# Optimization experiments

Hardware: AMD Instinct MI355X
Metric: run time of the kernel (lower is better)

The kernel has to match this reference:

```python
import jax, jax.numpy as jnp
import numpy as np

DIM = 1024
NUM_HEADS = 32
HEAD_DIM = 32
T = 2048
SCALE = 0.12
ROT_BASE = HEAD_DIM * 4  # Rotary(head_dim, max_seq_len, head_dim*4)
RMS_EPS = 1.1920929e-07  # torch float32 finfo eps (F.rms_norm default)


def _rms_norm(x):
    ms = jnp.mean(jnp.square(x), axis=-1, keepdims=True)
    return x * jax.lax.rsqrt(ms + RMS_EPS)


def _rotary_tables(seq_len):
    # modded-nanogpt half-truncated rotary: frequencies on first quarter, zeros on second
    quarter = HEAD_DIM // 4
    af = (1.0 / ROT_BASE) ** jnp.linspace(0.0, 1.0, quarter, dtype=jnp.float32)
    af = jnp.concatenate([af, jnp.zeros(quarter, dtype=jnp.float32)])  # [hd/2]
    theta = jnp.arange(seq_len, dtype=jnp.float32)[:, None] * af[None, :]  # [T, hd/2]
    return jnp.cos(theta), jnp.sin(theta)


def _apply_rotary(x, cos, sin):
    # x: [B, T, H, hd]; cos/sin: [T, hd/2]
    x1, x2 = jnp.split(x, 2, axis=-1)
    c = cos[None, :, None, :]
    s = sin[None, :, None, :]
    y1 = x1 * c + x2 * s
    y2 = -x1 * s + x2 * c
    return jnp.concatenate([y1, y2], axis=-1)


def setup_inputs() -> dict:
    key = jax.random.key(0)
    k1, k2, k3, k4 = jax.random.split(key, 4)
    std = 0.5 * DIM ** (-0.5)
    bound = (3.0 ** 0.5) * std
    x = jax.random.normal(k1, (1, T, DIM), dtype=jnp.float32)
    ve = jax.random.normal(k2, (1, T, NUM_HEADS * HEAD_DIM), dtype=jnp.float32)
    qkv_w = jax.random.uniform(k3, (3, NUM_HEADS * HEAD_DIM, DIM), dtype=jnp.float32,
                               minval=-bound, maxval=bound)
    lambdas = jnp.array([0.5, 0.5], dtype=jnp.float32)
    # original zero-inits c_proj; use small random so output/grads are nontrivial
    c_proj_w = jax.random.normal(k4, (DIM, NUM_HEADS * HEAD_DIM), dtype=jnp.float32) * 0.02
    return {"x": x, "ve": ve, "qkv_w": qkv_w, "lambdas": lambdas, "c_proj_w": c_proj_w}


def reference(x, ve, qkv_w, lambdas, c_proj_w):
    B, T_, D = x.shape
    H, hd = NUM_HEADS, HEAD_DIM
    # fused QKV projection: F.linear(x, qkv_w.flatten(end_dim=1))
    w = qkv_w.reshape(3 * H * hd, D)
    qkv = jnp.einsum('btd,ed->bte', x, w).reshape(B, T_, 3 * H, hd)
    q, k, v = jnp.split(qkv, 3, axis=2)  # each [B, T, H, hd]
    q = _rms_norm(q)
    k = _rms_norm(k)
    cos, sin = _rotary_tables(T_)
    q = _apply_rotary(q, cos, sin)
    k = _apply_rotary(k, cos, sin)
    v = lambdas[0] * v + lambdas[1] * ve.reshape(B, T_, H, hd)
    # causal attention with fixed scale 0.12
    scores = jnp.einsum('bqhd,bkhd->bhqk', q, k) * SCALE
    causal = jnp.tril(jnp.ones((T_, T_), dtype=bool))
    scores = jnp.where(causal[None, None, :, :], scores, -jnp.inf)
    attn = jax.nn.softmax(scores, axis=-1)
    y = jnp.einsum('bhqk,bkhd->bqhd', attn, v).reshape(B, T_, H * hd)
    return jnp.einsum('bte,de->btd', y, c_proj_w)
```

## Files before the change

kernel.cpp:

```cpp
#include <hip/hip_runtime.h>
#include <hip/hip_bf16.h>

#define NHEADS 32
#define HD_ 32
#define TSEQ 2048
#define SCALE_ 0.12f
#define LOG2E_ 1.44269504088896f
#define RMS_EPS_ 1.1920929e-07f

typedef unsigned short ushort_t;
typedef __bf16 bf16_t;
typedef __attribute__((ext_vector_type(8))) bf16_t bf16x8;
typedef __attribute__((ext_vector_type(4))) float f32x4;
typedef __attribute__((ext_vector_type(8))) unsigned short u16x8;

__device__ __forceinline__ ushort_t f2bfn(float f){
    __hip_bfloat16 b = __float2bfloat16(f);
    return *reinterpret_cast<ushort_t*>(&b);
}
__device__ __forceinline__ float bf2f(ushort_t s){
    union { unsigned u; float f; } v; v.u = ((unsigned)s) << 16;
    return v.f;
}
__device__ __forceinline__ float fexp2(float x){
#if __has_builtin(__builtin_amdgcn_exp2f)
    return __builtin_amdgcn_exp2f(x);
#else
    return exp2f(x);
#endif
}
__device__ __forceinline__ void gld16(const void* g, void* l){
    __builtin_amdgcn_global_load_lds(
        (const __attribute__((address_space(1))) unsigned int*)g,
        (__attribute__((address_space(3))) unsigned int*)l,
        16, 0, 0);
}

__global__ __launch_bounds__(256) void k_convert(const float* __restrict__ src,
                                                 ushort_t* __restrict__ dst, int n4){
    int i = blockIdx.x * blockDim.x + threadIdx.x;
    int stride = gridDim.x * blockDim.x;
    for (; i < n4; i += stride){
        float4 v = ((const float4*)src)[i];
        ushort4 o;
        o.x = f2bfn(v.x); o.y = f2bfn(v.y); o.z = f2bfn(v.z); o.w = f2bfn(v.w);
        ((ushort4*)dst)[i] = o;
    }
}

__global__ __launch_bounds__(256) void k_tables(float* __restrict__ cost, float* __restrict__ sint){
    int gid = blockIdx.x * 256 + threadIdx.x;
    if (gid >= TSEQ * 16) return;
    int t = gid >> 4, i = gid & 15;
    float c = 1.0f, s = 0.0f;
    if (i < 8){
        float af = powf(1.0f / 128.0f, (float)i * (1.0f / 7.0f));
        float th = (float)t * af;
        sincosf(th, &s, &c);
    }
    cost[gid] = c;
    sint[gid] = s;
}

template<int BM, int BN, bool OUT_BF16>
__global__ __launch_bounds__(256) void k_gemm64(const ushort_t* __restrict__ A,
                                                const ushort_t* __restrict__ B,
                                                void* __restrict__ C,
                                                int M, int N, int K)
{
    constexpr int MI = BM / 32, NI = BN / 32;
    __shared__ __align__(16) ushort_t As[BM * 64];
    __shared__ __align__(16) ushort_t Bs[BN * 64];
    const int tid = threadIdx.x;
    const int lane = tid & 63;
    const int w = tid >> 6;
    const int wr = w >> 1, wc = w & 1;
    const int l15 = lane & 15, hi = lane >> 4;
    const int m0 = blockIdx.y * BM, n0 = blockIdx.x * BN;
    const int srow = lane >> 3, scol = (lane & 7) * 8;

    f32x4 acc[MI][NI] = {};

    for (int k0 = 0; k0 < K; k0 += 64){
        __syncthreads();
        #pragma unroll
        for (int i = 0; i < BM / 32; ++i){
            int c = w * (BM / 32) + i;
            gld16(&A[(size_t)(m0 + c * 8 + srow) * K + k0 + scol], &As[c * 512]);
        }
        #pragma unroll
        for (int i = 0; i < BN / 32; ++i){
            int c = w * (BN / 32) + i;
            gld16(&B[(size_t)(n0 + c * 8 + srow) * K + k0 + scol], &Bs[c * 512]);
        }
        __syncthreads();
        bf16x8 af[MI][2], bfr[NI][2];
        #pragma unroll
        for (int mi = 0; mi < MI; ++mi)
            #pragma unroll
            for (int sub = 0; sub < 2; ++sub)
                af[mi][sub] = *(const bf16x8*)&As[(wr * (BM/2) + mi * 16 + l15) * 64 + sub * 32 + hi * 8];
        #pragma unroll
        for (int ni = 0; ni < NI; ++ni)
            #pragma unroll
            for (int sub = 0; sub < 2; ++sub)
                bfr[ni][sub] = *(const bf16x8*)&Bs[(wc * (BN/2) + ni * 16 + l15) * 64 + sub * 32 + hi * 8];
        #pragma unroll
        for (int sub = 0; sub < 2; ++sub)
            #pragma unroll
            for (int mi = 0; mi < MI; ++mi)
                #pragma unroll
                for (int ni = 0; ni < NI; ++ni)
                    acc[mi][ni] = __builtin_amdgcn_mfma_f32_16x16x32_bf16(af[mi][sub], bfr[ni][sub], acc[mi][ni], 0, 0, 0);
    }

    #pragma unroll
    for (int mi = 0; mi < MI; ++mi)
        #pragma unroll
        for (int ni = 0; ni < NI; ++ni)
            #pragma unroll
            for (int r = 0; r < 4; ++r){
                int row = m0 + wr * (BM/2) + mi * 16 + hi * 4 + r;
                int col = n0 + wc * (BN/2) + ni * 16 + l15;
                float v = acc[mi][ni][r];
                if (OUT_BF16) ((ushort_t*)C)[(size_t)row * N + col] = f2bfn(v);
                else          ((float*)C)[(size_t)row * N + col] = v;
            }
}

__global__ __launch_bounds__(256) void k_fuse(const ushort_t* __restrict__ qkvb,
                                              const float* __restrict__ ve,
                                              const float* __restrict__ lam,
                                              const float* __restrict__ cost,
                                              const float* __restrict__ sint,
                                              ushort_t* __restrict__ qb,
                                              ushort_t* __restrict__ kb,
                                              ushort_t* __restrict__ vtb)
{
    const int h  = blockIdx.y;
    const int t0 = blockIdx.x * 64;
    const int tid = threadIdx.x;
    const int tl = tid >> 2;
    const int dg = tid & 3;
    const int t  = t0 + tl;

    __shared__ __align__(16) float vtile[32 * 65];

    float cs[8], sn[8];
    #pragma unroll
    for (int j = 0; j < 8; ++j){
        int ci = (dg * 8 + j) & 15;
        cs[j] = cost[t * 16 + ci];
        sn[j] = sint[t * 16 + ci];
    }
    const float sgn = (dg < 2) ? 1.0f : -1.0f;

    #pragma unroll
    for (int which = 0; which < 2; ++which){
        u16x8 raw = *(const u16x8*)&qkvb[(size_t)t * 3072 + which * 1024 + h * 32 + dg * 8];
        float v[8];
        float ss = 0.0f;
        #pragma unroll
        for (int j = 0; j < 8; ++j){ v[j] = bf2f(raw[j]); ss += v[j] * v[j]; }
        ss += __shfl_xor(ss, 1);
        ss += __shfl_xor(ss, 2);
        const float inv = rsqrtf(ss * (1.0f / 32.0f) + RMS_EPS_);
        const float scl = (which == 0) ? SCALE_ * LOG2E_ : 1.0f;
        u16x8 o;
        #pragma unroll
        for (int j = 0; j < 8; ++j){
            float nv = v[j] * inv;
            float p  = __shfl_xor(nv, 2);
            o[j] = f2bfn((nv * cs[j] + sgn * p * sn[j]) * scl);
        }
        ushort_t* dst = (which == 0) ? qb : kb;
        *(u16x8*)&dst[((size_t)h * TSEQ + t) * 32 + dg * 8] = o;
    }

    const float l0 = lam[0], l1 = lam[1];
    {
        u16x8 raw = *(const u16x8*)&qkvb[(size_t)t * 3072 + 2048 + h * 32 + dg * 8];
        const float4* vep = (const float4*)&ve[(size_t)t * 1024 + h * 32 + dg * 8];
        float4 a = vep[0], b = vep[1];
        float vef[8] = {a.x, a.y, a.z, a.w, b.x, b.y, b.z, b.w};
        #pragma unroll
        for (int j = 0; j < 8; ++j)
            vtile[(dg * 8 + j) * 65 + tl] = l0 * bf2f(raw[j]) + l1 * vef[j];
    }
    __syncthreads();
    {
        const int d = tid >> 3, jj = tid & 7;
        u16x8 o;
        #pragma unroll
        for (int e = 0; e < 8; ++e)
            o[e] = f2bfn(vtile[d * 65 + jj * 8 + e]);
        *(u16x8*)&vtb[((size_t)h * HD_ + d) * TSEQ + t0 + jj * 8] = o;
    }
}

struct ChainState { f32x4 a0, a1; float m, lp; };

template<bool MASK>
__device__ __forceinline__ void attn_tile(const ushort_t* __restrict__ kb_h,
                                          const ushort_t* __restrict__ vt_h,
                                          ushort_t* pb, const bf16x8& qf,
                                          int kb0, int qglob, int l15, int hi,
                                          ChainState& st)
{
    bf16x8 vv0[2], vv1[2];
    #pragma unroll
    for (int kk = 0; kk < 2; ++kk){
        vv0[kk] = *(const bf16x8*)&vt_h[(size_t)l15 * TSEQ + kb0 + kk * 32 + hi * 8];
        vv1[kk] = *(const bf16x8*)&vt_h[(size_t)(16 + l15) * TSEQ + kb0 + kk * 32 + hi * 8];
    }
    f32x4 s[4];
    #pragma unroll
    for (int ni = 0; ni < 4; ++ni){
        bf16x8 kf = *(const bf16x8*)&kb_h[(size_t)(kb0 + ni * 16 + l15) * 32 + hi * 8];
        f32x4 z = {0.f, 0.f, 0.f, 0.f};
        s[ni] = __builtin_amdgcn_mfma_f32_16x16x32_bf16(kf, qf, z, 0, 0, 0);
    }
    if (MASK){
        #pragma unroll
        for (int ni = 0; ni < 4; ++ni)
            #pragma unroll
            for (int r = 0; r < 4; ++r)
                if (kb0 + ni * 16 + hi * 4 + r > qglob) s[ni][r] = -1e30f;
    }
    float mt = -1e30f;
    #pragma unroll
    for (int ni = 0; ni < 4; ++ni)
        #pragma unroll
        for (int r = 0; r < 4; ++r)
            mt = fmaxf(mt, s[ni][r]);
    mt = fmaxf(mt, __shfl_xor(mt, 16));
    mt = fmaxf(mt, __shfl_xor(mt, 32));
    float mn = fmaxf(st.m, mt);
    float sc = fexp2(st.m - mn);
    st.m = mn;
    float ps = 0.f;
    #pragma unroll
    for (int ni = 0; ni < 4; ++ni)
        #pragma unroll
        for (int r = 0; r < 4; ++r){
            float p = fexp2(s[ni][r] - mn);
            s[ni][r] = p;
            ps += p;
        }
    st.lp = st.lp * sc + ps;
    #pragma unroll
    for (int r = 0; r < 4; ++r){ st.a0[r] *= sc; st.a1[r] *= sc; }
    #pragma unroll
    for (int ni = 0; ni < 4; ++ni){
        ushort4 pk;
        pk.x = f2bfn(s[ni][0]); pk.y = f2bfn(s[ni][1]);
        pk.z = f2bfn(s[ni][2]); pk.w = f2bfn(s[ni][3]);
        *(ushort4*)&pb[l15 * 72 + ni * 16 + hi * 4] = pk;
    }
    #pragma unroll
    for (int kk = 0; kk < 2; ++kk){
        bf16x8 pf = *(const bf16x8*)&pb[l15 * 72 + kk * 32 + hi * 8];
        st.a0 = __builtin_amdgcn_mfma_f32_16x16x32_bf16(vv0[kk], pf, st.a0, 0, 0, 0);
        st.a1 = __builtin_amdgcn_mfma_f32_16x16x32_bf16(vv1[kk], pf, st.a1, 0, 0, 0);
    }
}

__device__ __forceinline__ void run_range(const ushort_t* kb_h, const ushort_t* vt_h,
                                          ushort_t* pb, const bf16x8& qf, int qglob,
                                          int lo, int hi_t, int nT, int l15, int hi,
                                          ChainState& st)
{
    int stop = (hi_t < nT) ? hi_t : (nT - 1);
    for (int kt = lo; kt < stop; ++kt)
        attn_tile<false>(kb_h, vt_h, pb, qf, kt * 64, qglob, l15, hi, st);
    if (hi_t == nT && lo < nT)
        attn_tile<true>(kb_h, vt_h, pb, qf, (nT - 1) * 64, qglob, l15, hi, st);
}

__device__ __forceinline__ void merge_state(ChainState& s, const float* mb){
    float m2 = mb[0];
    float mn = fmaxf(s.m, m2);
    float f1 = fexp2(s.m - mn), f2 = fexp2(m2 - mn);
    s.lp = s.lp * f1 + mb[1] * f2;
    #pragma unroll
    for (int r = 0; r < 4; ++r){
        s.a0[r] = s.a0[r] * f1 + mb[2 + r] * f2;
        s.a1[r] = s.a1[r] * f1 + mb[6 + r] * f2;
    }
    s.m = mn;
}

__global__ __launch_bounds__(512, 4) void k_attn(const ushort_t* __restrict__ qb,
                                                 const ushort_t* __restrict__ kb,
                                                 const ushort_t* __restrict__ vtb,
                                                 ushort_t* __restrict__ yb)
{
    const int h  = blockIdx.y;
    const int b  = blockIdx.x;
    const int tid = threadIdx.x;
    const int w = tid >> 6, lane = tid & 63;
    const int ws = w & 3, half2 = w >> 2;
    const int l15 = lane & 15, hi = lane >> 4;

    __shared__ __align__(16) ushort_t Pall[8][16 * 72];
    __shared__ float mbuf[4][64][20];
    ushort_t* pb = &Pall[w][0];

    const ushort_t* kb_h = kb + (size_t)h * TSEQ * HD_;
    const ushort_t* vt_h = vtb + (size_t)h * HD_ * TSEQ;
    const ushort_t* qb_h = qb + (size_t)h * TSEQ * HD_;

    const int qtA = b, qtB = 31 - b;
    const int nA = qtA + 1, nB = qtB + 1;
    const int hA = (nA + 1) >> 1, hB = nB >> 1;

    const int qwA = qtA * 64 + ws * 16;
    const int qwB = qtB * 64 + ws * 16;
    const bf16x8 qfA = *(const bf16x8*)&qb_h[(size_t)(qwA + l15) * 32 + hi * 8];
    const bf16x8 qfB = *(const bf16x8*)&qb_h[(size_t)(qwB + l15) * 32 + hi * 8];

    ChainState stA, stB;
    stA.a0 = {0.f,0.f,0.f,0.f}; stA.a1 = {0.f,0.f,0.f,0.f}; stA.m = -1e30f; stA.lp = 0.f;
    stB = stA;

    if (half2 == 0){
        run_range(kb_h, vt_h, pb, qfA, qwA + l15, 0, hA, nA, l15, hi, stA);
        run_range(kb_h, vt_h, pb, qfB, qwB + l15, 0, hB, nB, l15, hi, stB);
    } else {
        run_range(kb_h, vt_h, pb, qfA, qwA + l15, hA, nA, nA, l15, hi, stA);
        run_range(kb_h, vt_h, pb, qfB, qwB + l15, hB, nB, nB, l15, hi, stB);
    }

    if (half2 == 1){
        float* mb = &mbuf[ws][lane][0];
        mb[0] = stA.m; mb[1] = stA.lp;
        #pragma unroll
        for (int r = 0; r < 4; ++r){ mb[2 + r] = stA.a0[r]; mb[6 + r] = stA.a1[r]; }
        mb[10] = stB.m; mb[11] = stB.lp;
        #pragma unroll
        for (int r = 0; r < 4; ++r){ mb[12 + r] = stB.a0[r]; mb[16 + r] = stB.a1[r]; }
    }
    __syncthreads();
    if (half2 == 0){
        merge_state(stA, &mbuf[ws][lane][0]);
        merge_state(stB, &mbuf[ws][lane][10]);
        #pragma unroll
        for (int which = 0; which < 2; ++which){
            ChainState& st = which ? stB : stA;
            int qw = which ? qwB : qwA;
            float ls = st.lp;
            ls += __shfl_xor(ls, 16);
            ls += __shfl_xor(ls, 32);
            float inv = 1.0f / ls;
            ushort4 o0, o1;
            o0.x = f2bfn(st.a0[0]*inv); o0.y = f2bfn(st.a0[1]*inv);
            o0.z = f2bfn(st.a0[2]*inv); o0.w = f2bfn(st.a0[3]*inv);
            o1.x = f2bfn(st.a1[0]*inv); o1.y = f2bfn(st.a1[1]*inv);
            o1.z = f2bfn(st.a1[2]*inv); o1.w = f2bfn(st.a1[3]*inv);
            size_t base = (size_t)(qw + l15) * 1024 + h * 32;
            *(ushort4*)&yb[base + hi * 4]      = o0;
            *(ushort4*)&yb[base + 16 + hi * 4] = o1;
        }
    }
}

extern "C" void kernel_launch(void* const* d_in, const int* in_sizes, int n_in,
                              void* d_out, int out_size, void* d_ws, size_t ws_size,
                              hipStream_t stream)
{
    const float* x   = (const float*)d_in[0];
    const float* ve  = (const float*)d_in[1];
    const float* qkw = (const float*)d_in[2];
    const float* lam = (const float*)d_in[3];
    const float* cpw = (const float*)d_in[4];

    char* ws = (char*)d_ws;
    size_t o = 0;
    auto take = [&](size_t bytes) -> char* {
        char* p = ws + o; o += (bytes + 255) & ~(size_t)255; return p;
    };
    ushort_t* xb   = (ushort_t*)take((size_t)TSEQ * 1024 * 2);
    ushort_t* wb   = (ushort_t*)take((size_t)3072 * 1024 * 2);
    ushort_t* cpb  = (ushort_t*)take((size_t)1024 * 1024 * 2);
    ushort_t* qkvb = (ushort_t*)take((size_t)TSEQ * 3072 * 2);
    float*    cost = (float*)take((size_t)TSEQ * 16 * 4);
    float*    sint = (float*)take((size_t)TSEQ * 16 * 4);
    ushort_t* qb   = (ushort_t*)take((size_t)NHEADS * TSEQ * HD_ * 2);
    ushort_t* kb   = (ushort_t*)take((size_t)NHEADS * TSEQ * HD_ * 2);
    ushort_t* vtb  = (ushort_t*)take((size_t)NHEADS * HD_ * TSEQ * 2);
    ushort_t* yb   = xb;

    k_convert<<<512, 256, 0, stream>>>(x,   xb,  TSEQ * 1024 / 4);
    k_convert<<<768, 256, 0, stream>>>(qkw, wb,  3072 * 1024 / 4);
    k_convert<<<256, 256, 0, stream>>>(cpw, cpb, 1024 * 1024 / 4);
    k_tables<<<TSEQ * 16 / 256, 256, 0, stream>>>(cost, sint);
    k_gemm64<64, 128, true ><<<dim3(3072 / 128, TSEQ / 64), 256, 0, stream>>>(xb, wb, qkvb, TSEQ, 3072, 1024);
    k_fuse<<<dim3(TSEQ / 64, NHEADS), 256, 0, stream>>>(qkvb, ve, lam, cost, sint, qb, kb, vtb);
    k_attn<<<dim3(16, NHEADS), 512, 0, stream>>>(qb, kb, vtb, yb);
    k_gemm64<64, 64, false><<<dim3(1024 / 64, TSEQ / 64), 256, 0, stream>>>(yb, cpb, (float*)d_out, TSEQ, 1024, 1024);
}
```

Baseline: 182.0 us.

## Restructure attention with LDS-staged K/V, fuse prep kernels, double-buffer GEMM

The attention kernel drops the split-range, 512-thread design and its cross-wave merge step. Each 256-thread block now streams K and V tiles through swizzled, double-buffered LDS via global_load_lds, and both query chains (tiles b and 31-b) share each staged tile. The online-softmax running max is removed, which relies on RMS-normed q/k and the fixed scale keeping exponents bounded. Blocks are remapped so the heads spread across XCDs. Separately, the three convert kernels and the rotary-table kernel are merged into one launch, and the GEMM gets a two-stage LDS prefetch; the cost is more LDS use and reliance on bounded scores for numerical safety.

Measured after the change: 161.5 us. 1.13x faster.

```diff
diff --git a/kernel.cpp b/kernel.cpp
--- a/kernel.cpp
+++ b/kernel.cpp
@@ -36,30 +36,38 @@
         16, 0, 0);
 }
 
-__global__ __launch_bounds__(256) void k_convert(const float* __restrict__ src,
-                                                 ushort_t* __restrict__ dst, int n4){
-    int i = blockIdx.x * blockDim.x + threadIdx.x;
-    int stride = gridDim.x * blockDim.x;
-    for (; i < n4; i += stride){
-        float4 v = ((const float4*)src)[i];
+__global__ __launch_bounds__(256) void k_prep(const float* __restrict__ x,
+                                              const float* __restrict__ qkw,
+                                              const float* __restrict__ cpw,
+                                              ushort_t* __restrict__ xb,
+                                              ushort_t* __restrict__ wb,
+                                              ushort_t* __restrict__ cpb,
+                                              float* __restrict__ cost,
+                                              float* __restrict__ sint)
+{
+    const int n1 = TSEQ * 1024 / 4, n2 = 3 * 1024 * 1024 / 4, n3 = 1024 * 1024 / 4;
+    int i = blockIdx.x * 256 + threadIdx.x;
+    if (i < n1 + n2 + n3){
+        const float* src; ushort_t* dst; int j = i;
+        if (j < n1){ src = x; dst = xb; }
+        else if (j < n1 + n2){ j -= n1; src = qkw; dst = wb; }
+        else { j -= n1 + n2; src = cpw; dst = cpb; }
+        float4 v = ((const float4*)src)[j];
         ushort4 o;
         o.x = f2bfn(v.x); o.y = f2bfn(v.y); o.z = f2bfn(v.z); o.w = f2bfn(v.w);
-        ((ushort4*)dst)[i] = o;
-    }
-}
-
-__global__ __launch_bounds__(256) void k_tables(float* __restrict__ cost, float* __restrict__ sint){
-    int gid = blockIdx.x * 256 + threadIdx.x;
-    if (gid >= TSEQ * 16) return;
-    int t = gid >> 4, i = gid & 15;
-    float c = 1.0f, s = 0.0f;
-    if (i < 8){
-        float af = powf(1.0f / 128.0f, (float)i * (1.0f / 7.0f));
-        float th = (float)t * af;
-        sincosf(th, &s, &c);
-    }
-    cost[gid] = c;
-    sint[gid] = s;
+        ((ushort4*)dst)[j] = o;
+    } else {
+        int g = i - (n1 + n2 + n3);
+        if (g < TSEQ * 16){
+            int t = g >> 4, ii = g & 15;
+            float c = 1.0f, s = 0.0f;
+            if (ii < 8){
+                float af = powf(1.0f / 128.0f, (float)ii * (1.0f / 7.0f));
+                sincosf((float)t * af, &s, &c);
+            }
+            cost[g] = c; sint[g] = s;
+        }
+    }
 }
 
 template<int BM, int BN, bool OUT_BF16>
@@ -69,8 +77,8 @@
                                                 int M, int N, int K)
 {
     constexpr int MI = BM / 32, NI = BN / 32;
-    __shared__ __align__(16) ushort_t As[BM * 64];
-    __shared__ __align__(16) ushort_t Bs[BN * 64];
+    __shared__ __align__(16) ushort_t As[2][BM * 64];
+    __shared__ __align__(16) ushort_t Bs[2][BN * 64];
     const int tid = threadIdx.x;
     const int lane = tid & 63;
     const int w = tid >> 6;
@@ -81,30 +89,35 @@
 
     f32x4 acc[MI][NI] = {};
 
+    auto stage = [&](int k0, int buf){
+        #pragma unroll
+        for (int i = 0; i < BM / 32; ++i){
+            int c = w * (BM / 32) + i;
+            gld16(&A[(size_t)(m0 + c * 8 + srow) * K + k0 + scol], &As[buf][c * 512]);
+        }
+        #pragma unroll
+        for (int i = 0; i < BN / 32; ++i){
+            int c = w * (BN / 32) + i;
+            gld16(&B[(size_t)(n0 + c * 8 + srow) * K + k0 + scol], &Bs[buf][c * 512]);
+        }
+    };
+
+    stage(0, 0);
+    int cur = 0;
     for (int k0 = 0; k0 < K; k0 += 64){
         __syncthreads();
-        #pragma unroll
-        for (int i = 0; i < BM / 32; ++i){
-            int c = w * (BM / 32) + i;
-            gld16(&A[(size_t)(m0 + c * 8 + srow) * K + k0 + scol], &As[c * 512]);
-        }
-        #pragma unroll
-        for (int i = 0; i < BN / 32; ++i){
-            int c = w * (BN / 32) + i;
-            gld16(&B[(size_t)(n0 + c * 8 + srow) * K + k0 + scol], &Bs[c * 512]);
-        }
-        __syncthreads();
+        if (k0 + 64 < K) stage(k0 + 64, cur ^ 1);
         bf16x8 af[MI][2], bfr[NI][2];
         #pragma unroll
         for (int mi = 0; mi < MI; ++mi)
             #pragma unroll
             for (int sub = 0; sub < 2; ++sub)
-                af[mi][sub] = *(const bf16x8*)&As[(wr * (BM/2) + mi * 16 + l15) * 64 + sub * 32 + hi * 8];
+                af[mi][sub] = *(const bf16x8*)&As[cur][(wr * (BM/2) + mi * 16 + l15) * 64 + sub * 32 + hi * 8];
         #pragma unroll
         for (int ni = 0; ni < NI; ++ni)
             #pragma unroll
             for (int sub = 0; sub < 2; ++sub)
-                bfr[ni][sub] = *(const bf16x8*)&Bs[(wc * (BN/2) + ni * 16 + l15) * 64 + sub * 32 + hi * 8];
+                bfr[ni][sub] = *(const bf16x8*)&Bs[cur][(wc * (BN/2) + ni * 16 + l15) * 64 + sub * 32 + hi * 8];
         #pragma unroll
         for (int sub = 0; sub < 2; ++sub)
             #pragma unroll
@@ -112,6 +125,7 @@
                 #pragma unroll
                 for (int ni = 0; ni < NI; ++ni)
                     acc[mi][ni] = __builtin_amdgcn_mfma_f32_16x16x32_bf16(af[mi][sub], bfr[ni][sub], acc[mi][ni], 0, 0, 0);
+        cur ^= 1;
     }
 
     #pragma unroll
@@ -198,58 +212,36 @@
     }
 }
 
-struct ChainState { f32x4 a0, a1; float m, lp; };
-
 template<bool MASK>
-__device__ __forceinline__ void attn_tile(const ushort_t* __restrict__ kb_h,
-                                          const ushort_t* __restrict__ vt_h,
-                                          ushort_t* pb, const bf16x8& qf,
-                                          int kb0, int qglob, int l15, int hi,
-                                          ChainState& st)
-{
-    bf16x8 vv0[2], vv1[2];
-    #pragma unroll
-    for (int kk = 0; kk < 2; ++kk){
-        vv0[kk] = *(const bf16x8*)&vt_h[(size_t)l15 * TSEQ + kb0 + kk * 32 + hi * 8];
-        vv1[kk] = *(const bf16x8*)&vt_h[(size_t)(16 + l15) * TSEQ + kb0 + kk * 32 + hi * 8];
-    }
+__device__ __forceinline__ void chain_step(const bf16x8* kf, const bf16x8* vv0, const bf16x8* vv1,
+                                           ushort_t* pb, const bf16x8& qf,
+                                           int kb0, int qrow, int l15, int hi,
+                                           f32x4& a0, f32x4& a1, float& lp)
+{
     f32x4 s[4];
     #pragma unroll
     for (int ni = 0; ni < 4; ++ni){
-        bf16x8 kf = *(const bf16x8*)&kb_h[(size_t)(kb0 + ni * 16 + l15) * 32 + hi * 8];
         f32x4 z = {0.f, 0.f, 0.f, 0.f};
-        s[ni] = __builtin_amdgcn_mfma_f32_16x16x32_bf16(kf, qf, z, 0, 0, 0);
+        s[ni] = __builtin_amdgcn_mfma_f32_16x16x32_bf16(kf[ni], qf, z, 0, 0, 0);
     }
     if (MASK){
+        const int relc = qrow - kb0 - 4 * hi;
         #pragma unroll
         for (int ni = 0; ni < 4; ++ni)
             #pragma unroll
             for (int r = 0; r < 4; ++r)
-                if (kb0 + ni * 16 + hi * 4 + r > qglob) s[ni][r] = -1e30f;
-    }
-    float mt = -1e30f;
+                if (16 * ni + r > relc) s[ni][r] = -1e30f;
+    }
+    float ps = 0.f;
     #pragma unroll
     for (int ni = 0; ni < 4; ++ni)
         #pragma unroll
-        for (int r = 0; r < 4; ++r)
-            mt = fmaxf(mt, s[ni][r]);
-    mt = fmaxf(mt, __shfl_xor(mt, 16));
-    mt = fmaxf(mt, __shfl_xor(mt, 32));
-    float mn = fmaxf(st.m, mt);
-    float sc = fexp2(st.m - mn);
-    st.m = mn;
-    float ps = 0.f;
-    #pragma unroll
-    for (int ni = 0; ni < 4; ++ni)
-        #pragma unroll
         for (int r = 0; r < 4; ++r){
-            float p = fexp2(s[ni][r] - mn);
+            float p = fexp2(s[ni][r]);
             s[ni][r] = p;
             ps += p;
         }
-    st.lp = st.lp * sc + ps;
-    #pragma unroll
-    for (int r = 0; r < 4; ++r){ st.a0[r] *= sc; st.a1[r] *= sc; }
+    lp += ps;
     #pragma unroll
     for (int ni = 0; ni < 4; ++ni){
         ushort4 pk;
@@ -260,107 +252,100 @@
     #pragma unroll
     for (int kk = 0; kk < 2; ++kk){
         bf16x8 pf = *(const bf16x8*)&pb[l15 * 72 + kk * 32 + hi * 8];
-        st.a0 = __builtin_amdgcn_mfma_f32_16x16x32_bf16(vv0[kk], pf, st.a0, 0, 0, 0);
-        st.a1 = __builtin_amdgcn_mfma_f32_16x16x32_bf16(vv1[kk], pf, st.a1, 0, 0, 0);
-    }
-}
-
-__device__ __forceinline__ void run_range(const ushort_t* kb_h, const ushort_t* vt_h,
-                                          ushort_t* pb, const bf16x8& qf, int qglob,
-                                          int lo, int hi_t, int nT, int l15, int hi,
-                                          ChainState& st)
-{
-    int stop = (hi_t < nT) ? hi_t : (nT - 1);
-    for (int kt = lo; kt < stop; ++kt)
-        attn_tile<false>(kb_h, vt_h, pb, qf, kt * 64, qglob, l15, hi, st);
-    if (hi_t == nT && lo < nT)
-        attn_tile<true>(kb_h, vt_h, pb, qf, (nT - 1) * 64, qglob, l15, hi, st);
-}
-
-__device__ __forceinline__ void merge_state(ChainState& s, const float* mb){
-    float m2 = mb[0];
-    float mn = fmaxf(s.m, m2);
-    float f1 = fexp2(s.m - mn), f2 = fexp2(m2 - mn);
-    s.lp = s.lp * f1 + mb[1] * f2;
-    #pragma unroll
-    for (int r = 0; r < 4; ++r){
-        s.a0[r] = s.a0[r] * f1 + mb[2 + r] * f2;
-        s.a1[r] = s.a1[r] * f1 + mb[6 + r] * f2;
-    }
-    s.m = mn;
-}
-
-__global__ __launch_bounds__(512, 4) void k_attn(const ushort_t* __restrict__ qb,
-                                                 const ushort_t* __restrict__ kb,
-                                                 const ushort_t* __restrict__ vtb,
-                                                 ushort_t* __restrict__ yb)
-{
-    const int h  = blockIdx.y;
-    const int b  = blockIdx.x;
+        a0 = __builtin_amdgcn_mfma_f32_16x16x32_bf16(vv0[kk], pf, a0, 0, 0, 0);
+        a1 = __builtin_amdgcn_mfma_f32_16x16x32_bf16(vv1[kk], pf, a1, 0, 0, 0);
+    }
+}
+
+__global__ __launch_bounds__(256) void k_attn(const ushort_t* __restrict__ qb,
+                                              const ushort_t* __restrict__ kb,
+                                              const ushort_t* __restrict__ vtb,
+                                              ushort_t* __restrict__ yb)
+{
+    const int bid = blockIdx.x;
+    const int xcd = bid & 7, idx = bid >> 3;
+    const int h = xcd * 4 + (idx >> 4);
+    const int b = idx & 15;
     const int tid = threadIdx.x;
     const int w = tid >> 6, lane = tid & 63;
-    const int ws = w & 3, half2 = w >> 2;
     const int l15 = lane & 15, hi = lane >> 4;
 
-    __shared__ __align__(16) ushort_t Pall[8][16 * 72];
-    __shared__ float mbuf[4][64][20];
-    ushort_t* pb = &Pall[w][0];
+    __shared__ __align__(16) ushort_t Kbuf[2][64 * 32];
+    __shared__ __align__(16) ushort_t Vbuf[2][32 * 64];
+    __shared__ __align__(16) ushort_t Pbuf[4][2][16 * 72];
 
     const ushort_t* kb_h = kb + (size_t)h * TSEQ * HD_;
     const ushort_t* vt_h = vtb + (size_t)h * HD_ * TSEQ;
     const ushort_t* qb_h = qb + (size_t)h * TSEQ * HD_;
 
     const int qtA = b, qtB = 31 - b;
-    const int nA = qtA + 1, nB = qtB + 1;
-    const int hA = (nA + 1) >> 1, hB = nB >> 1;
-
-    const int qwA = qtA * 64 + ws * 16;
-    const int qwB = qtB * 64 + ws * 16;
+    const int qwA = qtA * 64 + w * 16, qwB = qtB * 64 + w * 16;
     const bf16x8 qfA = *(const bf16x8*)&qb_h[(size_t)(qwA + l15) * 32 + hi * 8];
     const bf16x8 qfB = *(const bf16x8*)&qb_h[(size_t)(qwB + l15) * 32 + hi * 8];
 
-    ChainState stA, stB;
-    stA.a0 = {0.f,0.f,0.f,0.f}; stA.a1 = {0.f,0.f,0.f,0.f}; stA.m = -1e30f; stA.lp = 0.f;
-    stB = stA;
-
-    if (half2 == 0){
-        run_range(kb_h, vt_h, pb, qfA, qwA + l15, 0, hA, nA, l15, hi, stA);
-        run_range(kb_h, vt_h, pb, qfB, qwB + l15, 0, hB, nB, l15, hi, stB);
-    } else {
-        run_range(kb_h, vt_h, pb, qfA, qwA + l15, hA, nA, nA, l15, hi, stA);
-        run_range(kb_h, vt_h, pb, qfB, qwB + l15, hB, nB, nB, l15, hi, stB);
-    }
-
-    if (half2 == 1){
-        float* mb = &mbuf[ws][lane][0];
-        mb[0] = stA.m; mb[1] = stA.lp;
-        #pragma unroll
-        for (int r = 0; r < 4; ++r){ mb[2 + r] = stA.a0[r]; mb[6 + r] = stA.a1[r]; }
-        mb[10] = stB.m; mb[11] = stB.lp;
-        #pragma unroll
-        for (int r = 0; r < 4; ++r){ mb[12 + r] = stB.a0[r]; mb[16 + r] = stB.a1[r]; }
-    }
-    __syncthreads();
-    if (half2 == 0){
-        merge_state(stA, &mbuf[ws][lane][0]);
-        merge_state(stB, &mbuf[ws][lane][10]);
-        #pragma unroll
-        for (int which = 0; which < 2; ++which){
-            ChainState& st = which ? stB : stA;
-            int qw = which ? qwB : qwA;
-            float ls = st.lp;
-            ls += __shfl_xor(ls, 16);
-            ls += __shfl_xor(ls, 32);
-            float inv = 1.0f / ls;
-            ushort4 o0, o1;
-            o0.x = f2bfn(st.a0[0]*inv); o0.y = f2bfn(st.a0[1]*inv);
-            o0.z = f2bfn(st.a0[2]*inv); o0.w = f2bfn(st.a0[3]*inv);
-            o1.x = f2bfn(st.a1[0]*inv); o1.y = f2bfn(st.a1[1]*inv);
-            o1.z = f2bfn(st.a1[2]*inv); o1.w = f2bfn(st.a1[3]*inv);
-            size_t base = (size_t)(qw + l15) * 1024 + h * 32;
-            *(ushort4*)&yb[base + hi * 4]      = o0;
-            *(ushort4*)&yb[base + 16 + hi * 4] = o1;
-        }
+    const int krow_in = w * 16 + (lane >> 2);
+    const int kslot_in = (lane & 3) ^ ((krow_in >> 1) & 3);
+    const int vrow_in = w * 8 + (lane >> 3);
+    const int vslot_in = (lane & 7) ^ (vrow_in & 7);
+
+    auto stage = [&](int kt, int buf){
+        int kb0 = kt * 64;
+        gld16(&kb_h[(size_t)(kb0 + krow_in) * 32 + kslot_in * 8], &Kbuf[buf][w * 512]);
+        gld16(&vt_h[(size_t)vrow_in * TSEQ + kb0 + vslot_in * 8], &Vbuf[buf][w * 512]);
+    };
+
+    const int kswz = hi ^ ((l15 >> 1) & 3);
+    const int vswz = l15 & 7;
+
+    f32x4 a0A = {0.f,0.f,0.f,0.f}, a1A = a0A, a0B = a0A, a1B = a0A;
+    float lpA = 0.f, lpB = 0.f;
+    ushort_t* pbB = &Pbuf[w][0][0];
+    ushort_t* pbA = &Pbuf[w][1][0];
+
+    stage(0, 0);
+    int cur = 0;
+    const int nB = qtB + 1;
+    for (int kt = 0; kt < nB; ++kt){
+        __syncthreads();
+        if (kt + 1 < nB) stage(kt + 1, cur ^ 1);
+        const int kb0 = kt * 64;
+        bf16x8 kf[4], vv0[2], vv1[2];
+        #pragma unroll
+        for (int ni = 0; ni < 4; ++ni)
+            kf[ni] = *(const bf16x8*)&Kbuf[cur][(16 * ni + l15) * 32 + kswz * 8];
+        #pragma unroll
+        for (int kk = 0; kk < 2; ++kk){
+            vv0[kk] = *(const bf16x8*)&Vbuf[cur][l15 * 64 + ((kk * 4 + hi) ^ vswz) * 8];
+            vv1[kk] = *(const bf16x8*)&Vbuf[cur][(16 + l15) * 64 + ((kk * 4 + hi) ^ vswz) * 8];
+        }
+        if (kt < qtB)
+            chain_step<false>(kf, vv0, vv1, pbB, qfB, kb0, qwB + l15, l15, hi, a0B, a1B, lpB);
+        else
+            chain_step<true >(kf, vv0, vv1, pbB, qfB, kb0, qwB + l15, l15, hi, a0B, a1B, lpB);
+        if (kt < qtA)
+            chain_step<false>(kf, vv0, vv1, pbA, qfA, kb0, qwA + l15, l15, hi, a0A, a1A, lpA);
+        else if (kt == qtA)
+            chain_step<true >(kf, vv0, vv1, pbA, qfA, kb0, qwA + l15, l15, hi, a0A, a1A, lpA);
+        cur ^= 1;
+    }
+
+    #pragma unroll
+    for (int which = 0; which < 2; ++which){
+        f32x4 a0 = which ? a0B : a0A;
+        f32x4 a1 = which ? a1B : a1A;
+        float lp = which ? lpB : lpA;
+        int qw = which ? qwB : qwA;
+        lp += __shfl_xor(lp, 16);
+        lp += __shfl_xor(lp, 32);
+        float inv = 1.0f / lp;
+        ushort4 o0, o1;
+        o0.x = f2bfn(a0[0]*inv); o0.y = f2bfn(a0[1]*inv);
+        o0.z = f2bfn(a0[2]*inv); o0.w = f2bfn(a0[3]*inv);
+        o1.x = f2bfn(a1[0]*inv); o1.y = f2bfn(a1[1]*inv);
+        o1.z = f2bfn(a1[2]*inv); o1.w = f2bfn(a1[3]*inv);
+        size_t base = (size_t)(qw + l15) * 1024 + h * 32;
+        *(ushort4*)&yb[base + hi * 4]      = o0;
+        *(ushort4*)&yb[base + 16 + hi * 4] = o1;
     }
 }
 
@@ -390,12 +375,10 @@
     ushort_t* vtb  = (ushort_t*)take((size_t)NHEADS * HD_ * TSEQ * 2);
     ushort_t* yb   = xb;
 
-    k_convert<<<512, 256, 0, stream>>>(x,   xb,  TSEQ * 1024 / 4);
-    k_convert<<<768, 256, 0, stream>>>(qkw, wb,  3072 * 1024 / 4);
-    k_convert<<<256, 256, 0, stream>>>(cpw, cpb, 1024 * 1024 / 4);
-    k_tables<<<TSEQ * 16 / 256, 256, 0, stream>>>(cost, sint);
+    const int prep_items = (TSEQ * 1024 + 3 * 1024 * 1024 + 1024 * 1024) / 4 + TSEQ * 16;
+    k_prep<<<(prep_items + 255) / 256, 256, 0, stream>>>(x, qkw, cpw, xb, wb, cpb, cost, sint);
     k_gemm64<64, 128, true ><<<dim3(3072 / 128, TSEQ / 64), 256, 0, stream>>>(xb, wb, qkvb, TSEQ, 3072, 1024);
     k_fuse<<<dim3(TSEQ / 64, NHEADS), 256, 0, stream>>>(qkvb, ve, lam, cost, sint, qb, kb, vtb);
-    k_attn<<<dim3(16, NHEADS), 512, 0, stream>>>(qb, kb, vtb, yb);
+    k_attn<<<512, 256, 0, stream>>>(qb, kb, vtb, yb);
     k_gemm64<64, 64, false><<<dim3(1024 / 64, TSEQ / 64), 256, 0, stream>>>(yb, cpb, (float*)d_out, TSEQ, 1024, 1024);
 }
```
